# Kernel tuning notes

Hardware: AMD Instinct MI355X
Metric: run time of the kernel (lower is better)

Reference implementation:

```python
import jax, jax.numpy as jnp
import numpy as np

T, B, IN, OUT, N_MODULES, K = 2048, 8, 1024, 1024, 16, 2


def setup_inputs() -> dict:
    key = jax.random.key(0)
    k1, k2, k3 = jax.random.split(key, 3)
    x = jax.random.normal(k1, (T, B, IN), dtype=jnp.float32)          # time-major input
    selection = jax.random.randint(k2, (B, K), 0, N_MODULES, dtype=jnp.int32)
    # kaiming-uniform-ish scale for [n_modules, out, in] weight
    bound = 1.0 / np.sqrt(IN)
    weight = jax.random.uniform(k3, (N_MODULES, OUT, IN), dtype=jnp.float32,
                                minval=-bound, maxval=bound)
    return {"x": x, "selection": selection, "weight": weight}


def reference(x, selection, weight):
    # Faithful to ModularLinear.forward with time_major=True, sum_outputs=False, bias=None.
    # Original computes o = x @ all-expert weights -> [B, n_modules, T, out], then for each
    # selection column i gathers o[b, selection[b, i]] and concats on the last dim.
    # Equivalent math: gather the selected expert weights per (batch, slot) and do one GEMM.
    # x: [T, B, in]; selection: [B, K]; weight: [n_modules, out, in]
    w_sel = weight[selection]                              # [B, K, out, in]
    o = jnp.einsum('tbi,bkoi->tbko', x, w_sel)             # [T, B, K, out]
    t, b, k, d = o.shape
    return o.reshape(t, b, k * d)                          # [T, B, K*out]
```

## Files before the change

### kernel.cpp

```cpp
#include <hip/hip_runtime.h>

#define T_DIM   2048
#define B_DIM   8
#define IN_DIM  1024
#define OUT_DIM 1024
#define NMOD    16
#define KSLOT   2

#define BM 128
#define BN 128
#define BK 32

typedef __bf16 bf16x8 __attribute__((ext_vector_type(8)));
typedef float  f32x4  __attribute__((ext_vector_type(4)));

typedef const __attribute__((address_space(1))) void* gptr_t;
typedef __attribute__((address_space(3))) void* lptr_t;

__device__ __forceinline__ void async_load16(const void* gp, void* lp) {
  __builtin_amdgcn_global_load_lds((gptr_t)gp, (lptr_t)lp, 16, 0, 0);
}

__device__ __forceinline__ unsigned short f2bf_rne(float f) {
  unsigned int u = __float_as_uint(f);
  u += 0x7fffu + ((u >> 16) & 1u);
  return (unsigned short)(u >> 16);
}

__global__ __launch_bounds__(256) void convert_repack(
    const float* __restrict__ x, const float* __restrict__ w,
    unsigned short* __restrict__ xb, unsigned short* __restrict__ wb) {
  long tid = (long)blockIdx.x * blockDim.x + threadIdx.x;
  const long XCH = (long)T_DIM * B_DIM * IN_DIM / 4;
  if (tid < XCH) {
    float4 v = ((const float4*)x)[tid];
    long e = tid << 2;
    int  i = (int)(e & (IN_DIM - 1));
    long tb = e >> 10;
    int  b = (int)(tb & (B_DIM - 1));
    long t = tb >> 3;
    ushort4 o;
    o.x = f2bf_rne(v.x); o.y = f2bf_rne(v.y); o.z = f2bf_rne(v.z); o.w = f2bf_rne(v.w);
    *(ushort4*)(xb + (((long)b * T_DIM + t) << 10) + i) = o;
  } else {
    long c = tid - XCH;
    float4 v = ((const float4*)w)[c];
    ushort4 o;
    o.x = f2bf_rne(v.x); o.y = f2bf_rne(v.y); o.z = f2bf_rne(v.z); o.w = f2bf_rne(v.w);
    ((ushort4*)wb)[c] = o;
  }
}

__global__ __launch_bounds__(256) void gemm_mod(
    const unsigned short* __restrict__ xb, const unsigned short* __restrict__ wb,
    const int* __restrict__ sel, float* __restrict__ out) {
  __shared__ alignas(16) unsigned short As[BM * BK];
  __shared__ alignas(16) unsigned short Bs[BN * BK];

  const int nt = blockIdx.x;
  const int mt = blockIdx.y;
  const int bk = blockIdx.z;
  const int b  = bk >> 1;
  const int ks = bk & 1;
  const int expert = sel[bk];

  const unsigned short* A  = xb + ((long)b * T_DIM + (long)mt * BM) * IN_DIM;
  const unsigned short* Bw = wb + ((long)expert * OUT_DIM + (long)nt * BN) * IN_DIM;

  const int tid  = threadIdx.x;
  const int lane = tid & 63;
  const int c0 = tid, c1 = tid + 256;

  const int lm = lane & 15;
  const int kg = lane >> 4;

  const int wave = tid >> 6;
  const int wm = (wave >> 1) * 64;
  const int wn = (wave & 1) * 64;

  f32x4 acc[4][4];
  const f32x4 z = {0.f, 0.f, 0.f, 0.f};
  #pragma unroll
  for (int i = 0; i < 4; ++i)
    #pragma unroll
    for (int j = 0; j < 4; ++j) acc[i][j] = z;

  const long ga0 = (long)(c0 >> 2) * IN_DIM + (c0 & 3) * 8;
  const long ga1 = (long)(c1 >> 2) * IN_DIM + (c1 & 3) * 8;

  for (int kt = 0; kt < IN_DIM; kt += BK) {
    __syncthreads();
    async_load16(A  + ga0 + kt, &As[c0 * 8]);
    async_load16(A  + ga1 + kt, &As[c1 * 8]);
    async_load16(Bw + ga0 + kt, &Bs[c0 * 8]);
    async_load16(Bw + ga1 + kt, &Bs[c1 * 8]);
    __syncthreads();

    bf16x8 af[4], bfr[4];
    #pragma unroll
    for (int mi = 0; mi < 4; ++mi)
      af[mi] = *(const bf16x8*)&As[(wm + mi * 16 + lm) * BK + kg * 8];
    #pragma unroll
    for (int ni = 0; ni < 4; ++ni)
      bfr[ni] = *(const bf16x8*)&Bs[(wn + ni * 16 + lm) * BK + kg * 8];

    #pragma unroll
    for (int mi = 0; mi < 4; ++mi)
      #pragma unroll
      for (int ni = 0; ni < 4; ++ni)
        acc[mi][ni] = __builtin_amdgcn_mfma_f32_16x16x32_bf16(af[mi], bfr[ni], acc[mi][ni], 0, 0, 0);
  }

  const int row0 = mt * BM + wm + kg * 4;
  const int col0 = nt * BN + wn + lm;
  #pragma unroll
  for (int mi = 0; mi < 4; ++mi) {
    #pragma unroll
    for (int r = 0; r < 4; ++r) {
      const int t = row0 + mi * 16 + r;
      float* po = out + (long)t * (B_DIM * KSLOT * OUT_DIM)
                      + b * (KSLOT * OUT_DIM) + ks * OUT_DIM + col0;
      #pragma unroll
      for (int ni = 0; ni < 4; ++ni)
        po[ni * 16] = acc[mi][ni][r];
    }
  }
}

extern "C" void kernel_launch(void* const* d_in, const int* in_sizes, int n_in,
                              void* d_out, int out_size, void* d_ws, size_t ws_size,
                              hipStream_t stream) {
  const float* x   = (const float*)d_in[0];
  const int*   sel = (const int*)d_in[1];
  const float* w   = (const float*)d_in[2];
  float* out = (float*)d_out;

  unsigned short* xb = (unsigned short*)d_ws;
  unsigned short* wb = xb + (long)T_DIM * B_DIM * IN_DIM;

  const long total_chunks =
      ((long)T_DIM * B_DIM * IN_DIM + (long)NMOD * OUT_DIM * IN_DIM) / 4;
  dim3 cgrid((unsigned)((total_chunks + 255) / 256));
  convert_repack<<<cgrid, 256, 0, stream>>>(x, w, xb, wb);

  dim3 ggrid(OUT_DIM / BN, T_DIM / BM, B_DIM * KSLOT);
  gemm_mod<<<ggrid, 256, 0, stream>>>(xb, wb, sel, out);
}
```

Measured before the change: 334.3 us.

## Drop x transpose in conversion, read strided A, swizzle LDS tiles

The conversion kernel no longer repacks x into batch-major order. It becomes a plain contiguous fp32-to-bf16 cast that processes 8 elements per thread with a single 16-byte store. The GEMM now reads A rows directly from the time-major layout with a stride of B*IN. Both LDS tiles get an XOR swizzle on the 16-byte chunk index to reduce bank conflicts on fragment reads. The aim is to save conversion write traffic and shared-memory conflicts, at the cost of strided global reads for A in the GEMM.

```diff
diff --git a/kernel.cpp b/kernel.cpp
--- a/kernel.cpp
+++ b/kernel.cpp
@@ -13,6 +13,7 @@
 
 typedef __bf16 bf16x8 __attribute__((ext_vector_type(8)));
 typedef float  f32x4  __attribute__((ext_vector_type(4)));
+typedef unsigned short ushort8 __attribute__((ext_vector_type(8)));
 
 typedef const __attribute__((address_space(1))) void* gptr_t;
 typedef __attribute__((address_space(3))) void* lptr_t;
@@ -27,28 +28,22 @@
   return (unsigned short)(u >> 16);
 }
 
-__global__ __launch_bounds__(256) void convert_repack(
+__global__ __launch_bounds__(256) void convert_bf16(
     const float* __restrict__ x, const float* __restrict__ w,
     unsigned short* __restrict__ xb, unsigned short* __restrict__ wb) {
-  long tid = (long)blockIdx.x * blockDim.x + threadIdx.x;
-  const long XCH = (long)T_DIM * B_DIM * IN_DIM / 4;
-  if (tid < XCH) {
-    float4 v = ((const float4*)x)[tid];
-    long e = tid << 2;
-    int  i = (int)(e & (IN_DIM - 1));
-    long tb = e >> 10;
-    int  b = (int)(tb & (B_DIM - 1));
-    long t = tb >> 3;
-    ushort4 o;
-    o.x = f2bf_rne(v.x); o.y = f2bf_rne(v.y); o.z = f2bf_rne(v.z); o.w = f2bf_rne(v.w);
-    *(ushort4*)(xb + (((long)b * T_DIM + t) << 10) + i) = o;
-  } else {
-    long c = tid - XCH;
-    float4 v = ((const float4*)w)[c];
-    ushort4 o;
-    o.x = f2bf_rne(v.x); o.y = f2bf_rne(v.y); o.z = f2bf_rne(v.z); o.w = f2bf_rne(v.w);
-    ((ushort4*)wb)[c] = o;
-  }
+  const long tid = (long)blockIdx.x * blockDim.x + threadIdx.x;
+  const long XV = (long)T_DIM * B_DIM * IN_DIM / 8;
+  const float4* src;
+  unsigned short* dst;
+  long v;
+  if (tid < XV) { v = tid;      src = (const float4*)x; dst = xb; }
+  else          { v = tid - XV; src = (const float4*)w; dst = wb; }
+  float4 a = src[2 * v];
+  float4 c = src[2 * v + 1];
+  ushort8 o;
+  o[0] = f2bf_rne(a.x); o[1] = f2bf_rne(a.y); o[2] = f2bf_rne(a.z); o[3] = f2bf_rne(a.w);
+  o[4] = f2bf_rne(c.x); o[5] = f2bf_rne(c.y); o[6] = f2bf_rne(c.z); o[7] = f2bf_rne(c.w);
+  *(ushort8*)(dst + v * 8) = o;
 }
 
 __global__ __launch_bounds__(256) void gemm_mod(
@@ -64,15 +59,24 @@
   const int ks = bk & 1;
   const int expert = sel[bk];
 
-  const unsigned short* A  = xb + ((long)b * T_DIM + (long)mt * BM) * IN_DIM;
+  const int AS = B_DIM * IN_DIM;
+  const unsigned short* A  = xb + ((long)mt * BM * B_DIM + b) * IN_DIM;
   const unsigned short* Bw = wb + ((long)expert * OUT_DIM + (long)nt * BN) * IN_DIM;
 
   const int tid  = threadIdx.x;
   const int lane = tid & 63;
   const int c0 = tid, c1 = tid + 256;
 
+  const int r0 = c0 >> 2, g0 = (c0 & 3) ^ ((r0 >> 2) & 3);
+  const int r1 = c1 >> 2, g1 = (c1 & 3) ^ ((r1 >> 2) & 3);
+  const long a0 = (long)r0 * AS + g0 * 8;
+  const long a1 = (long)r1 * AS + g1 * 8;
+  const long b0 = (long)r0 * IN_DIM + g0 * 8;
+  const long b1 = (long)r1 * IN_DIM + g1 * 8;
+
   const int lm = lane & 15;
   const int kg = lane >> 4;
+  const int ksw = ((kg ^ ((lm >> 2) & 3))) * 8;
 
   const int wave = tid >> 6;
   const int wm = (wave >> 1) * 64;
@@ -85,24 +89,21 @@
     #pragma unroll
     for (int j = 0; j < 4; ++j) acc[i][j] = z;
 
-  const long ga0 = (long)(c0 >> 2) * IN_DIM + (c0 & 3) * 8;
-  const long ga1 = (long)(c1 >> 2) * IN_DIM + (c1 & 3) * 8;
-
   for (int kt = 0; kt < IN_DIM; kt += BK) {
     __syncthreads();
-    async_load16(A  + ga0 + kt, &As[c0 * 8]);
-    async_load16(A  + ga1 + kt, &As[c1 * 8]);
-    async_load16(Bw + ga0 + kt, &Bs[c0 * 8]);
-    async_load16(Bw + ga1 + kt, &Bs[c1 * 8]);
+    async_load16(A  + a0 + kt, &As[c0 * 8]);
+    async_load16(A  + a1 + kt, &As[c1 * 8]);
+    async_load16(Bw + b0 + kt, &Bs[c0 * 8]);
+    async_load16(Bw + b1 + kt, &Bs[c1 * 8]);
     __syncthreads();
 
     bf16x8 af[4], bfr[4];
     #pragma unroll
     for (int mi = 0; mi < 4; ++mi)
-      af[mi] = *(const bf16x8*)&As[(wm + mi * 16 + lm) * BK + kg * 8];
+      af[mi] = *(const bf16x8*)&As[(wm + mi * 16 + lm) * BK + ksw];
     #pragma unroll
     for (int ni = 0; ni < 4; ++ni)
-      bfr[ni] = *(const bf16x8*)&Bs[(wn + ni * 16 + lm) * BK + kg * 8];
+      bfr[ni] = *(const bf16x8*)&Bs[(wn + ni * 16 + lm) * BK + ksw];
 
     #pragma unroll
     for (int mi = 0; mi < 4; ++mi)
@@ -138,10 +139,10 @@
   unsigned short* xb = (unsigned short*)d_ws;
   unsigned short* wb = xb + (long)T_DIM * B_DIM * IN_DIM;
 
-  const long total_chunks =
-      ((long)T_DIM * B_DIM * IN_DIM + (long)NMOD * OUT_DIM * IN_DIM) / 4;
-  dim3 cgrid((unsigned)((total_chunks + 255) / 256));
-  convert_repack<<<cgrid, 256, 0, stream>>>(x, w, xb, wb);
+  const long total_vecs =
+      ((long)T_DIM * B_DIM * IN_DIM + (long)NMOD * OUT_DIM * IN_DIM) / 8;
+  dim3 cgrid((unsigned)((total_vecs + 255) / 256));
+  convert_bf16<<<cgrid, 256, 0, stream>>>(x, w, xb, wb);
 
   dim3 ggrid(OUT_DIM / BN, T_DIM / BM, B_DIM * KSLOT);
   gemm_mod<<<ggrid, 256, 0, stream>>>(xb, wb, sel, out);
```

Result: no change. 334.7 us (+0.1%).
